# Optimization experiments

Hardware: AMD Instinct MI355X
Metric: run time of the kernel (lower is better)

The kernel has to match this reference:

```python
import jax, jax.numpy as jnp
from jax import lax
import numpy as np

# HH / synapse constants (CFG in original repo; standard values matching the rate eqns)
GNA, GK, GL = 40.0, 35.0, 0.3
ENA, EK, EL = 55.0, -77.0, -65.0
GS, VS = 1.0, 0.0
IAPP = 1.0
VT, KP = -20.0, 3.0
A_D, A_R = 1.0, 0.1
DT = 0.02

B, N, L = 16, 2000, 1024


def setup_inputs() -> dict:
    key = jax.random.key(0)
    z = jax.random.uniform(key, (B, N, L), dtype=jnp.float32)
    return {"z": z}


def _rates(V):
    # Singularity-safe rate constants (the torch code patches V==25 / V==-35 exactly).
    at25 = V == 25.0
    atm35 = V == -35.0
    dN = jnp.where(at25, 1.0, 1.0 - jnp.exp((-V + 25.0) / 9.0))
    dM = jnp.where(atm35, 1.0, 1.0 - jnp.exp((-V - 35.0) / 9.0))
    dNb = jnp.where(at25, 1.0, 1.0 - jnp.exp((V - 25.0) / 9.0))
    dMb = jnp.where(atm35, 1.0, 1.0 - jnp.exp((V + 35.0) / 9.0))
    aN = jnp.where(at25, 0.18, 0.02 * (V - 25.0) / dN)
    bN = jnp.where(at25, 0.08, -0.002 * (V - 25.0) / dNb)
    aM = jnp.where(atm35, 1.638, 0.182 * (V + 35.0) / dM)
    bM = jnp.where(atm35, 1.16, -0.124 * (V + 35.0) / dMb)
    aH = 0.25 * jnp.exp((-V - 90.0) / 12.0)
    bH = 0.25 * jnp.exp((V + 34.0) / 12.0)
    return aN, bN, aM, bM, aH, bH


def _step(carry, z_prev):
    V, m, n, h, y = carry
    pow1 = GNA * m ** 3 * h
    pow2 = GK * n ** 4
    G = DT / 2 * (pow1 + pow2 + GL + GS * y)
    E = pow1 * ENA + pow2 * EK + GL * EL + GS * VS * y
    Vn = (V * (1.0 - G) + DT * (E + IAPP)) / (1.0 + G)
    aN, bN, aM, bM, aH, bH = _rates(Vn)
    mn = (aM * DT + (1.0 - DT / 2 * (aM + bM)) * m) / (DT / 2 * (aM + bM) + 1.0)
    nn = (aN * DT + (1.0 - DT / 2 * (aN + bN)) * n) / (DT / 2 * (aN + bN) + 1.0)
    hn = (aH * DT + (1.0 - DT / 2 * (aH + bH)) * h) / (DT / 2 * (aH + bH) + 1.0)
    ady = A_D * z_prev
    yn = (ady * DT + (1.0 - DT / 2 * (ady + A_R)) * y) / (DT / 2 * (ady + A_R) + 1.0)
    return (Vn, mn, nn, hn, yn), Vn


def _hh(z):
    b, n_t, l = z.shape
    zt = jnp.moveaxis(z, 1, 0)  # (N, B, L); step k uses z[k-1]
    V0 = jnp.full((b, l), -70.0, dtype=z.dtype)
    zeros = jnp.zeros((b, l), dtype=z.dtype)
    ones = jnp.ones((b, l), dtype=z.dtype)
    carry0 = (V0, zeros, zeros, ones, zeros)
    _, Vseq = lax.scan(_step, carry0, zt[:-1])  # (N-1, B, L)
    Vall = jnp.concatenate([V0[None], Vseq], axis=0)  # (N, B, L)
    V = jnp.moveaxis(Vall, 0, 1)  # (B, N, L)
    return jax.nn.sigmoid((V - VT) / KP)


def reference(z):
    return _hh(z)
```

## Files before the change

### kernel.cpp

```cpp
#include <hip/hip_runtime.h>

#define N_ 2000
#define L_ 1024

__device__ __forceinline__ float rcpf(float d) { return __builtin_amdgcn_rcpf(d); }
__device__ __forceinline__ float ex2(float x)  { return __builtin_amdgcn_exp2f(x); }

__device__ __forceinline__ float dppx1(float x) {
    return __int_as_float(
        __builtin_amdgcn_mov_dpp(__float_as_int(x), 0xB1, 0xF, 0xF, true));
}

#define STEP2(K, RS, DOSTORE)                                                 \
  {                                                                           \
    const int kk = (K);                                                       \
    float zc = zb[RS];                                                        \
    int kpre = kk + 7;                                                        \
    int kc = kpre < 1998 ? kpre : 1998;                                       \
    zb[RS] = z[base + kc * L_];                                               \
                             \
    float w    = evn ? sB : sA;                                               \
    float t1   = sA * sA;                                                     \
    float val  = (t1 * sA) * w;                                               \
    float gAdd = evn ? 0.003f : 0.01f * sB;               \
    float Gh   = __fmaf_rn(val, cG, gAdd);                                    \
    float Eh   = __fmaf_rn(val, cE, eAdd);                                    \
    float G    = Gh + dppx1(Gh);                                              \
    float E    = Eh + dppx1(Eh);                                              \
    float num  = __fmaf_rn(V, 1.0f - G, __fmaf_rn(E, 0.02f, 0.02f));          \
    float Vn   = num * rcpf(1.0f + G);                                        \
        \
    float eR   = ex2(__fmaf_rn(Vn, K9, cX));                                  \
    float u    = Vn + cu;                                                     \
    float r    = rcpf(eR - 1.0f);                                             \
    float ur   = u * r;                                                       \
    bool  pat  = (Vn == cc);                                                  \
    float av   = pat ? pa  : ka * (ur * eR);                                  \
    float s1   = pat ? cs1 : ur * __fmaf_rn(ka01, eR, kb01);                  \
      \
    float vH   = 0.25f * ex2(__fmaf_rn(Vn, sHc, cHc));                        \
    float vHx  = dppx1(vH);                                                   \
                                         \
    float q1   = 1.0f + s1;                                                   \
    float num1 = __fmaf_rn(av, 0.02f, __fmaf_rn(-s1, sA, sA));                \
                                         \
    float a2   = evn ? vH  : zc;                                              \
    float b2   = evn ? vHx : 0.1f;                                            \
    float s2   = __fmaf_rn(a2, 0.01f, 0.01f * b2);                            \
    float q2   = 1.0f + s2;                                                   \
    float num2 = __fmaf_rn(a2, 0.02f, __fmaf_rn(-s2, sB, sB));                \
    float rq   = rcpf(q1 * q2);                                               \
    sA = num1 * (rq * q2);                                                    \
    sB = num2 * (rq * q1);                                                    \
    V = Vn;                                                                   \
    if (DOSTORE) {                                                            \
         \
          \
      float esel = evn ? eRp : eR;                                            \
      float e3 = (esel * esel) * esel;                                        \
      float ts = e3 * C15L;                                                   \
      float sg = ts * rcpf(1.0f + ts);                                        \
      out[base + (kk - 1 + sub) * L_] = sg;                                   \
    } else {                                                                  \
      eRp = eR;                                                               \
    }                                                                         \
  }

__global__ __launch_bounds__(64) void hh_kernel(const float* __restrict__ z,
                                                float* __restrict__ out) {
    const int t   = blockIdx.x * 64 + threadIdx.x;
    const int sub = t & 1;
    const int ch  = t >> 1;
    const int b   = ch >> 10;
    const int l   = ch & 1023;
    const int base = b * (N_ * L_) + l;

    const bool evn = (sub == 0);

    const float K9  = 0.16029944898766259f;
    const float K12 = 0.12022458674074695f;

    const float cG   = evn ? 0.4f      : 0.35f;
    const float cE   = evn ? 2200.0f   : -2695.0f;
    const float eAdd = evn ? -19.5f    : 0.0f;
    const float cu   = evn ? 35.0f     : -25.0f;
    const float cX   = evn ? 35.0f*K9  : -25.0f*K9;
    const float cc   = evn ? -35.0f    : 25.0f;
    const float ka   = evn ? 0.182f    : 0.02f;
    const float ka01 = evn ? 0.00182f  : 0.0002f;
    const float kb01 = evn ? 0.00124f  : 0.00002f;
    const float pa   = evn ? 1.638f    : 0.18f;
    const float cs1  = evn ? 0.02798f  : 0.0026f;
    const float sHc  = evn ? -K12      : K12;
    const float cHc  = evn ? -90.0f*K12 : 34.0f*K12;
    const float C15L = evn ? 0.006737946999085467f
                           : 3269017.372472110639f;

    float V  = -70.0f;
    float sA = 0.0f;
    float sB = evn ? 1.0f : 0.0f;
    float eRp = ex2((-70.0f + 35.0f) * K9);

    float zb[8];
#pragma unroll
    for (int i = 0; i < 8; ++i) zb[i] = z[base + i * L_];

    int k2 = 1;
    for (int g = 0; g < 249; ++g) {
#pragma unroll
        for (int j = 0; j < 4; ++j) {
            STEP2(k2 + 2 * j,     2 * j,     true)
            STEP2(k2 + 2 * j + 1, 2 * j + 1, false)
        }
        k2 += 8;
    }
#pragma unroll
    for (int j = 0; j < 3; ++j) {
        STEP2(k2 + 2 * j,     2 * j,     true)
        STEP2(k2 + 2 * j + 1, 2 * j + 1, false)
    }
    STEP2(1999, 6, true)
}

extern "C" void kernel_launch(void* const* d_in, const int* in_sizes, int n_in,
                              void* d_out, int out_size, void* d_ws, size_t ws_size,
                              hipStream_t stream) {
    const float* z = (const float*)d_in[0];
    float* out = (float*)d_out;
    hh_kernel<<<512, 64, 0, stream>>>(z, out);
}
```

Measured before the change: 500.2 us.

## Process two batch channels per thread to interleave independent recurrences

Each thread now advances two independent HH recurrences (batches b and b+8) with their steps interleaved, and the grid is halved. The intent is to hide the latency of the serial rcp/exp/DPP dependency chain through instruction-level parallelism. In exchange, each CU gets fewer waves (only one wave per CU on 256 CUs) and register pressure roughly doubles, which can leave SIMDs idle.

```diff
diff --git a/kernel.cpp b/kernel.cpp
--- a/kernel.cpp
+++ b/kernel.cpp
@@ -11,13 +11,13 @@
         __builtin_amdgcn_mov_dpp(__float_as_int(x), 0xB1, 0xF, 0xF, true));
 }
 
-#define STEP2(K, RS, DOSTORE)                                                 \
+#define STEP2(V, sA, sB, eRp, zb, basev, K, RS, DOSTORE)                      \
   {                                                                           \
     const int kk = (K);                                                       \
     float zc = zb[RS];                                                        \
     int kpre = kk + 7;                                                        \
     int kc = kpre < 1998 ? kpre : 1998;                                       \
-    zb[RS] = z[base + kc * L_];                                               \
+    zb[RS] = z[basev + kc * L_];                                              \
                              \
     float w    = evn ? sB : sA;                                               \
     float t1   = sA * sA;                                                     \
@@ -55,12 +55,11 @@
     V = Vn;                                                                   \
     if (DOSTORE) {                                                            \
          \
-          \
       float esel = evn ? eRp : eR;                                            \
       float e3 = (esel * esel) * esel;                                        \
-      float ts = e3 * C15L;                                                   \
+      float ts = e3 * C15L;                              \
       float sg = ts * rcpf(1.0f + ts);                                        \
-      out[base + (kk - 1 + sub) * L_] = sg;                                   \
+      out[basev + (kk - 1 + sub) * L_] = sg;                                  \
     } else {                                                                  \
       eRp = eR;                                                               \
     }                                                                         \
@@ -73,7 +72,8 @@
     const int ch  = t >> 1;
     const int b   = ch >> 10;
     const int l   = ch & 1023;
-    const int base = b * (N_ * L_) + l;
+    const int baseA = b * (N_ * L_) + l;
+    const int baseB = baseA + 8 * (N_ * L_);
 
     const bool evn = (sub == 0);
 
@@ -96,30 +96,41 @@
     const float C15L = evn ? 0.006737946999085467f
                            : 3269017.372472110639f;
 
-    float V  = -70.0f;
-    float sA = 0.0f;
-    float sB = evn ? 1.0f : 0.0f;
-    float eRp = ex2((-70.0f + 35.0f) * K9);
+    float VA  = -70.0f;
+    float sAA = 0.0f;
+    float sBA = evn ? 1.0f : 0.0f;
+    float eRpA = ex2((-70.0f + 35.0f) * K9);
+    float VB  = -70.0f;
+    float sAB = 0.0f;
+    float sBB = evn ? 1.0f : 0.0f;
+    float eRpB = ex2((-70.0f + 35.0f) * K9);
 
-    float zb[8];
+    float zbA[8], zbB[8];
 #pragma unroll
-    for (int i = 0; i < 8; ++i) zb[i] = z[base + i * L_];
+    for (int i = 0; i < 8; ++i) zbA[i] = z[baseA + i * L_];
+#pragma unroll
+    for (int i = 0; i < 8; ++i) zbB[i] = z[baseB + i * L_];
 
     int k2 = 1;
     for (int g = 0; g < 249; ++g) {
 #pragma unroll
         for (int j = 0; j < 4; ++j) {
-            STEP2(k2 + 2 * j,     2 * j,     true)
-            STEP2(k2 + 2 * j + 1, 2 * j + 1, false)
+            STEP2(VA, sAA, sBA, eRpA, zbA, baseA, k2 + 2 * j,     2 * j,     true)
+            STEP2(VB, sAB, sBB, eRpB, zbB, baseB, k2 + 2 * j,     2 * j,     true)
+            STEP2(VA, sAA, sBA, eRpA, zbA, baseA, k2 + 2 * j + 1, 2 * j + 1, false)
+            STEP2(VB, sAB, sBB, eRpB, zbB, baseB, k2 + 2 * j + 1, 2 * j + 1, false)
         }
         k2 += 8;
     }
 #pragma unroll
     for (int j = 0; j < 3; ++j) {
-        STEP2(k2 + 2 * j,     2 * j,     true)
-        STEP2(k2 + 2 * j + 1, 2 * j + 1, false)
+        STEP2(VA, sAA, sBA, eRpA, zbA, baseA, k2 + 2 * j,     2 * j,     true)
+        STEP2(VB, sAB, sBB, eRpB, zbB, baseB, k2 + 2 * j,     2 * j,     true)
+        STEP2(VA, sAA, sBA, eRpA, zbA, baseA, k2 + 2 * j + 1, 2 * j + 1, false)
+        STEP2(VB, sAB, sBB, eRpB, zbB, baseB, k2 + 2 * j + 1, 2 * j + 1, false)
     }
-    STEP2(1999, 6, true)
+    STEP2(VA, sAA, sBA, eRpA, zbA, baseA, 1999, 6, true)
+    STEP2(VB, sAB, sBB, eRpB, zbB, baseB, 1999, 6, true)
 }
 
 extern "C" void kernel_launch(void* const* d_in, const int* in_sizes, int n_in,
@@ -127,5 +138,5 @@
                               hipStream_t stream) {
     const float* z = (const float*)d_in[0];
     float* out = (float*)d_out;
-    hh_kernel<<<512, 64, 0, stream>>>(z, out);
+    hh_kernel<<<256, 64, 0, stream>>>(z, out);
 }
```

Measured after the change: 659.3 us. 31.8% more time.
